# Optimization experiments

Measured on AMD Instinct MI355X. Metric: run time of the kernel, lower is better.

Reference implementation:

```python
import jax, jax.numpy as jnp
import numpy as np

N = 100000   # nodes
E = 3200000  # edges
F = 128      # num_features
H = 20       # hidden dim (hard-coded in source)
C = 10       # num_classes
EPS = 1e-5


def setup_inputs() -> dict:
    key = jax.random.key(0)
    ks = jax.random.split(key, 16)
    x = jax.random.normal(ks[0], (N, F), jnp.float32)
    edge_index = jax.random.randint(ks[1], (2, E), 0, N)
    edge_weights = jnp.ones((E,), jnp.float32)

    def lin_init(k, fan_in, shape):
        s = 1.0 / np.sqrt(fan_in)
        return jax.random.uniform(k, shape, jnp.float32, -s, s)

    return {
        "x": x,
        "edge_index": edge_index,
        "edge_weights": edge_weights,
        "W1": lin_init(ks[2], F, (F, H)), "b1": jnp.zeros((H,), jnp.float32),
        "g1": jnp.ones((H,), jnp.float32), "be1": jnp.zeros((H,), jnp.float32),
        "W2": lin_init(ks[3], H, (H, H)), "b2": jnp.zeros((H,), jnp.float32),
        "g2": jnp.ones((H,), jnp.float32), "be2": jnp.zeros((H,), jnp.float32),
        "W3": lin_init(ks[4], H, (H, H)), "b3": jnp.zeros((H,), jnp.float32),
        "Wl": lin_init(ks[5], 3 * H, (3 * H, C)), "bl": lin_init(ks[6], 3 * H, (C,)),
    }


def gcn_conv(x, src, dst, ew, W, b, n):
    # PyG GCNConv: transform, add self-loops, symmetric deg^-1/2 normalization, scatter-add.
    h = x @ W  # [N, out]
    loop = jnp.arange(n)
    src2 = jnp.concatenate([src, loop])
    dst2 = jnp.concatenate([dst, loop])
    ew2 = jnp.concatenate([ew, jnp.ones((n,), x.dtype)])
    deg = jax.ops.segment_sum(ew2, dst2, num_segments=n)
    dinv = jnp.where(deg > 0, jax.lax.rsqrt(deg), 0.0)
    coef = (dinv[src2] * ew2 * dinv[dst2])[:, None]  # [E+N, 1]
    out = jax.ops.segment_sum(h[src2] * coef, dst2, num_segments=n)
    return out + b


def batch_norm(x, g, b):
    m = x.mean(axis=0)
    v = x.var(axis=0)
    return (x - m) * jax.lax.rsqrt(v + EPS) * g + b


def reference(x, edge_index, edge_weights, W1, b1, g1, be1, W2, b2, g2, be2, W3, b3, Wl, bl):
    src, dst = edge_index[0], edge_index[1]
    n = x.shape[0]
    o1 = batch_norm(jax.nn.relu(gcn_conv(x, src, dst, edge_weights, W1, b1, n)), g1, be1)
    o2 = batch_norm(jax.nn.relu(gcn_conv(o1, src, dst, edge_weights, W2, b2, n)), g2, be2)
    o3 = jax.nn.relu(gcn_conv(o2, src, dst, edge_weights, W3, b3, n))
    emb = jnp.concatenate([o1, o2, o3], axis=1)  # [N, 60]
    return emb @ Wl + bl
```

## Files before the change

kernel.cpp:

```cpp
#include <hip/hip_runtime.h>
#include <hip/hip_fp16.h>


#define HD 20
#define EPS 1e-5f
#define BSH 7
#define NBMAX 1024
#define CAP 5632
#define CAPE 2816

typedef float __attribute__((ext_vector_type(4))) f4v;

__device__ __forceinline__ float4 ntld4(const float* p) {
    f4v v = __builtin_nontemporal_load((const f4v*)p);
    return make_float4(v.x, v.y, v.z, v.w);
}

__global__ __launch_bounds__(1024)
void init_kernel(int* bcnt, float* stats, float* zero20, int nbv) {
    int t = threadIdx.x;
    if (t < nbv) bcnt[t] = 0;
    if (t < 80) stats[t] = 0.0f;
    if (t < HD) zero20[t] = 0.0f;
}

__global__ __launch_bounds__(256)
void bucket_hist_kernel(const int* __restrict__ dst, int* __restrict__ bcnt,
                        int E, int chunk, int nbv) {
    __shared__ int lh[NBMAX];
    for (int i = threadIdx.x; i < nbv; i += 256) lh[i] = 0;
    __syncthreads();
    int s = blockIdx.x * chunk;
    int e = s + chunk; if (e > E) e = E;
    for (int j = s + threadIdx.x; j < e; j += 256)
        atomicAdd(&lh[dst[j] >> BSH], 1);
    __syncthreads();
    for (int i = threadIdx.x; i < nbv; i += 256)
        if (lh[i]) atomicAdd(&bcnt[i], lh[i]);
}

__global__ __launch_bounds__(1024)
void bucket_scan_kernel(const int* __restrict__ bcnt, int* __restrict__ bstart,
                        int* __restrict__ bcur, int* __restrict__ row_start,
                        int n, int E, int nbv) {
    __shared__ int s[1024];
    int t = threadIdx.x;
    int v = (t < nbv) ? bcnt[t] : 0;
    s[t] = v;
    __syncthreads();
    for (int off = 1; off < 1024; off <<= 1) {
        int u = (t >= off) ? s[t - off] : 0;
        __syncthreads();
        s[t] += u;
        __syncthreads();
    }
    if (t < nbv) { int st = s[t] - v; bstart[t] = st; bcur[t] = st; }
    if (t == 0) { bstart[nbv] = E; row_start[n] = E; }
}

__global__ __launch_bounds__(256)
void scatter_kernel(const int* __restrict__ src, const int* __restrict__ dst,
                    const float* __restrict__ ew, int* __restrict__ bcur,
                    int2* __restrict__ tmp, int E, int chunk, int nbv) {
    __shared__ int lh[NBMAX];
    __shared__ int lbase[NBMAX];
    for (int i = threadIdx.x; i < nbv; i += 256) lh[i] = 0;
    __syncthreads();
    int s = blockIdx.x * chunk;
    int e = s + chunk; if (e > E) e = E;
    for (int j = s + threadIdx.x; j < e; j += 256)
        atomicAdd(&lh[dst[j] >> BSH], 1);
    __syncthreads();
    for (int i = threadIdx.x; i < nbv; i += 256) {
        int c = lh[i];
        lbase[i] = c ? atomicAdd(&bcur[i], c) : 0;
        lh[i] = 0;
    }
    __syncthreads();
    for (int j = s + threadIdx.x; j < e; j += 256) {
        int d = dst[j];
        int b = d >> BSH;
        int pos = atomicAdd(&lh[b], 1);
        tmp[lbase[b] + pos] = make_int2(src[j] | ((d & ((1 << BSH) - 1)) << 20),
                                        __float_as_int(ew[j]));
    }
}

__global__ __launch_bounds__(256)
void finalize_kernel(const int2* __restrict__ tmp, const int* __restrict__ bstart,
                     int2* __restrict__ se, int* __restrict__ row_start,
                     float* __restrict__ dinv, int n) {
    __shared__ int hist[128];
    __shared__ float degs[128];
    __shared__ int off[128];
    __shared__ int cur[128];
    __shared__ int2 stage[CAP];
    int b = blockIdx.x;
    int s0 = bstart[b], s1 = bstart[b + 1];
    int cnt = s1 - s0;
    int t = threadIdx.x;
    if (t < 128) { hist[t] = 0; degs[t] = 0.0f; cur[t] = 0; }
    __syncthreads();
    for (int j = s0 + t; j < s1; j += 256) {
        int2 r = tmp[j];
        int l = r.x >> 20;
        atomicAdd(&hist[l], 1);
        atomicAdd(&degs[l], __int_as_float(r.y));
    }
    __syncthreads();
    if (t < 128) off[t] = hist[t];
    __syncthreads();
    for (int o = 1; o < 128; o <<= 1) {
        int u = (t < 128 && t >= o) ? off[t - o] : 0;
        __syncthreads();
        if (t < 128) off[t] += u;
        __syncthreads();
    }
    if (t < 128) {
        int node = (b << BSH) + t;
        if (node < n) {
            row_start[node] = s0 + off[t] - hist[t];
            dinv[node] = rsqrtf(1.0f + degs[t]);
        }
    }
    __syncthreads();
    if (cnt <= CAP) {
        for (int j = s0 + t; j < s1; j += 256) {
            int2 r = tmp[j];
            int l = r.x >> 20;
            int p = (off[l] - hist[l]) + atomicAdd(&cur[l], 1);
            stage[p] = make_int2(r.x & 0xFFFFF, r.y);
        }
        __syncthreads();
        for (int k = t; k < cnt; k += 256) se[s0 + k] = stage[k];
    } else {
        for (int j = s0 + t; j < s1; j += 256) {
            int2 r = tmp[j];
            int l = r.x >> 20;
            int p = (off[l] - hist[l]) + atomicAdd(&cur[l], 1);
            se[s0 + p] = make_int2(r.x & 0xFFFFF, r.y);
        }
    }
}

template<int FIN, int NPB>
__global__ __launch_bounds__(256)
void gemm_kernel(const float* __restrict__ in, const float* __restrict__ W,
                 const float* __restrict__ cvec, const float* __restrict__ dinv,
                 __half* __restrict__ hs, int n) {
    __shared__ float sWt[HD][FIN + 4];
    __shared__ float sIn[NPB][FIN + 4];
    __shared__ float sC[HD];
    for (int i = threadIdx.x; i < FIN * HD; i += 256) {
        int k = i / HD, f = i % HD;
        sWt[f][k] = W[i];
    }
    if (threadIdx.x < HD) sC[threadIdx.x] = cvec[threadIdx.x];
    int base = blockIdx.x * NPB;
    int nb = n - base; if (nb > NPB) nb = NPB;
    int lim = n * FIN;
    const int Q = FIN / 4;
    for (int i = threadIdx.x; i < NPB * Q; i += 256) {
        int row = i / Q, c = (i % Q) * 4;
        int g = (base + row) * FIN + c;
        *(float4*)&sIn[row][c] = (g < lim) ? ntld4(&in[g])
                                           : make_float4(0.f, 0.f, 0.f, 0.f);
    }
    __syncthreads();
    for (int idx = threadIdx.x; idx < NPB * HD; idx += 256) {
        int nl = idx / HD, f = idx % HD;
        float4 a = make_float4(0.f, 0.f, 0.f, 0.f);
        #pragma unroll 4
        for (int k = 0; k < FIN; k += 4) {
            float4 x4 = *(const float4*)&sIn[nl][k];
            float4 w4 = *(const float4*)&sWt[f][k];
            a.x = fmaf(x4.x, w4.x, a.x);
            a.y = fmaf(x4.y, w4.y, a.y);
            a.z = fmaf(x4.z, w4.z, a.z);
            a.w = fmaf(x4.w, w4.w, a.w);
        }
        if (nl < nb)
            hs[(size_t)(base + nl) * HD + f] = __float2half_rn(
                (((a.x + a.y) + (a.z + a.w)) + sC[f]) * dinv[base + nl]);
    }
}

#define FMA4(A, V, W) \
    A.x = fmaf(V.x, W, A.x); A.y = fmaf(V.y, W, A.y); \
    A.z = fmaf(V.z, W, A.z); A.w = fmaf(V.w, W, A.w);

__device__ __forceinline__ float4 h4f2(uint2 u) {
    float2 f0 = __half22float2(*reinterpret_cast<const __half2*>(&u.x));
    float2 f1 = __half22float2(*reinterpret_cast<const __half2*>(&u.y));
    return make_float4(f0.x, f0.y, f1.x, f1.y);
}

#define AGG_LOOP(EDGEAT)                                                     \
    {                                                                        \
        int2 e = EDGEAT(j);                                                  \
        float w = __int_as_float(e.y);                                       \
        const uint2* r = hs4 + (size_t)e.x * 5;                              \
        uint2 c0 = r[0], c1 = r[1], c2 = r[2], c3 = r[3], c4 = r[4];         \
        while (true) {                                                       \
            int jn = j + 4;                                                  \
            bool more = jn < s1;                                             \
            int jp = more ? jn : j;                                          \
            int2 en = EDGEAT(jp);                                            \
            const uint2* rn = hs4 + (size_t)en.x * 5;                        \
            uint2 n0 = rn[0], n1 = rn[1], n2 = rn[2], n3 = rn[3], n4 = rn[4];\
            float wn = __int_as_float(en.y);                                 \
            float4 v0 = h4f2(c0), v1 = h4f2(c1), v2 = h4f2(c2);              \
            float4 v3 = h4f2(c3), v4 = h4f2(c4);                             \
            FMA4(a0, v0, w) FMA4(a1, v1, w) FMA4(a2, v2, w)                  \
            FMA4(a3, v3, w) FMA4(a4, v4, w)                                  \
            if (!more) break;                                                \
            j = jn; w = wn;                                                  \
            c0 = n0; c1 = n1; c2 = n2; c3 = n3; c4 = n4;                     \
        }                                                                    \
    }

#define EDGE_LDS(jj) sse[(jj) - sb0]
#define EDGE_GBL(jj) se[(jj)]

template<int MODE>
__global__ __launch_bounds__(256)
void agg_kernel(const uint2* __restrict__ hs4, const float* __restrict__ dinv,
                const int* __restrict__ row_start, const int2* __restrict__ se,
                const float* __restrict__ bias, float* __restrict__ out,
                float* __restrict__ stat_sum, float* __restrict__ stat_sq,
                const float* __restrict__ o1, const float* __restrict__ o2,
                const float* __restrict__ Wlp, const float* __restrict__ blp,
                int n) {
    __shared__ int2 sse[CAPE];
    __shared__ float ls[HD], lq[HD];
    __shared__ float sW[600];
    __shared__ float sb[10];
    int base = blockIdx.x * 64;
    int nEnd = base + 64; if (nEnd > n) nEnd = n;
    int sb0 = row_start[base];
    int sb1 = row_start[nEnd];
    int span = sb1 - sb0;
    bool ok = (span <= CAPE);
    if (MODE == 0) {
        if (threadIdx.x < HD) { ls[threadIdx.x] = 0.0f; lq[threadIdx.x] = 0.0f; }
    } else {
        for (int i = threadIdx.x; i < 600; i += 256) sW[i] = Wlp[i];
        if (threadIdx.x < 10) sb[threadIdx.x] = blp[threadIdx.x];
    }
    if (ok) {
        for (int k = threadIdx.x; k < span; k += 256) {
            long long v = __builtin_nontemporal_load(
                (const long long*)(se + sb0 + k));
            sse[k] = *(const int2*)&v;
        }
    }
    __syncthreads();
    int i = base + (threadIdx.x >> 2), lane = threadIdx.x & 3;
    if (i < n) {
        float di = dinv[i];
        int s0 = row_start[i], s1 = row_start[i + 1];
        float4 a0, a1, a2, a3, a4;
        if (lane == 0) {
            const uint2* s = hs4 + (size_t)i * 5;
            a0 = h4f2(s[0]); a1 = h4f2(s[1]); a2 = h4f2(s[2]);
            a3 = h4f2(s[3]); a4 = h4f2(s[4]);
        } else {
            a0 = a1 = a2 = a3 = a4 = make_float4(0.f, 0.f, 0.f, 0.f);
        }
        int j = s0 + lane;
        if (j < s1) {
            if (ok) { AGG_LOOP(EDGE_LDS) }
            else    { AGG_LOOP(EDGE_GBL) }
        }
        #define REDX(A, M) \
            A.x += __shfl_xor(A.x, M); A.y += __shfl_xor(A.y, M); \
            A.z += __shfl_xor(A.z, M); A.w += __shfl_xor(A.w, M);
        #define RED4L(A) REDX(A, 1) REDX(A, 2)
        RED4L(a0) RED4L(a1) RED4L(a2) RED4L(a3) RED4L(a4)
        float4 acc[5] = {a0, a1, a2, a3, a4};
        float va[HD];
        #pragma unroll
        for (int q = 0; q < 5; ++q) {
            float4 bb = *(const float4*)(bias + 4 * q);
            va[4 * q + 0] = fmaxf(fmaf(acc[q].x, di, bb.x), 0.0f);
            va[4 * q + 1] = fmaxf(fmaf(acc[q].y, di, bb.y), 0.0f);
            va[4 * q + 2] = fmaxf(fmaf(acc[q].z, di, bb.z), 0.0f);
            va[4 * q + 3] = fmaxf(fmaf(acc[q].w, di, bb.w), 0.0f);
        }
        if (MODE == 0) {
            if (lane == 0) {
                #pragma unroll
                for (int q = 0; q < 5; ++q) {
                    ((float4*)out)[i * 5 + q] = make_float4(
                        va[4 * q], va[4 * q + 1], va[4 * q + 2], va[4 * q + 3]);
                    int f = 4 * q;
                    atomicAdd(&ls[f + 0], va[f + 0]); atomicAdd(&lq[f + 0], va[f + 0] * va[f + 0]);
                    atomicAdd(&ls[f + 1], va[f + 1]); atomicAdd(&lq[f + 1], va[f + 1] * va[f + 1]);
                    atomicAdd(&ls[f + 2], va[f + 2]); atomicAdd(&lq[f + 2], va[f + 2] * va[f + 2]);
                    atomicAdd(&ls[f + 3], va[f + 3]); atomicAdd(&lq[f + 3], va[f + 3] * va[f + 3]);
                }
            }
        } else {
            float r1[HD], r2[HD];
            #pragma unroll
            for (int q = 0; q < 5; ++q) {
                *(float4*)&r1[4 * q] = ((const float4*)(o1 + (size_t)i * HD))[q];
                *(float4*)&r2[4 * q] = ((const float4*)(o2 + (size_t)i * HD))[q];
            }
            for (int c = lane; c < 10; c += 4) {
                float s = sb[c];
                #pragma unroll
                for (int k = 0; k < HD; ++k) s = fmaf(r1[k], sW[k * 10 + c], s);
                #pragma unroll
                for (int k = 0; k < HD; ++k) s = fmaf(r2[k], sW[(HD + k) * 10 + c], s);
                #pragma unroll
                for (int k = 0; k < HD; ++k) s = fmaf(va[k], sW[(2 * HD + k) * 10 + c], s);
                out[(size_t)i * 10 + c] = s;
            }
        }
    }
    if (MODE == 0) {
        __syncthreads();
        if (threadIdx.x < HD) {
            atomicAdd(&stat_sum[threadIdx.x], ls[threadIdx.x]);
            atomicAdd(&stat_sq[threadIdx.x], lq[threadIdx.x]);
        }
    }
}

__global__ __launch_bounds__(512)
void bn_adjust_kernel(const float* __restrict__ sum, const float* __restrict__ sq,
                      const float* __restrict__ g, const float* __restrict__ be,
                      const float* __restrict__ W, float* __restrict__ scsh_out,
                      float* __restrict__ Wp, float* __restrict__ cvec, int n) {
    __shared__ float ssc[HD], ssh[HD];
    int t = threadIdx.x;
    if (t < HD) {
        float inv_n = 1.0f / (float)n;
        float m = sum[t] * inv_n;
        float var = sq[t] * inv_n - m * m;
        float sc = g[t] * rsqrtf(var + EPS);
        float sh = be[t] - m * sc;
        ssc[t] = sc; ssh[t] = sh;
        scsh_out[t] = sc; scsh_out[HD + t] = sh;
    }
    __syncthreads();
    if (t < HD * HD) Wp[t] = ssc[t / HD] * W[t];
    if (t < HD) {
        float acc = 0.0f;
        #pragma unroll
        for (int k = 0; k < HD; ++k) acc = fmaf(ssh[k], W[k * HD + t], acc);
        cvec[t] = acc;
    }
}

__global__ __launch_bounds__(640)
void bn_adjust2_kernel(const float* __restrict__ sum, const float* __restrict__ sq,
                       const float* __restrict__ g, const float* __restrict__ be,
                       const float* __restrict__ W, float* __restrict__ scsh_out,
                       float* __restrict__ Wp, float* __restrict__ cvec,
                       const float* __restrict__ Wl, const float* __restrict__ bl,
                       const float* __restrict__ scsh1,
                       float* __restrict__ Wlp, float* __restrict__ blp, int n) {
    __shared__ float ssc[HD], ssh[HD];
    int t = threadIdx.x;
    if (t < HD) {
        float inv_n = 1.0f / (float)n;
        float m = sum[t] * inv_n;
        float var = sq[t] * inv_n - m * m;
        float sc = g[t] * rsqrtf(var + EPS);
        float sh = be[t] - m * sc;
        ssc[t] = sc; ssh[t] = sh;
        scsh_out[t] = sc; scsh_out[HD + t] = sh;
    }
    __syncthreads();
    if (t < HD * HD) Wp[t] = ssc[t / HD] * W[t];
    if (t < HD) {
        float acc = 0.0f;
        #pragma unroll
        for (int k = 0; k < HD; ++k) acc = fmaf(ssh[k], W[k * HD + t], acc);
        cvec[t] = acc;
    }
    if (t < 600) {
        int k = t / 10;
        float s = (k < HD) ? scsh1[k] : (k < 2 * HD) ? ssc[k - HD] : 1.0f;
        Wlp[t] = s * Wl[t];
    }
    if (t < 10) {
        float acc = bl[t];
        #pragma unroll
        for (int k = 0; k < HD; ++k) acc = fmaf(scsh1[HD + k], Wl[k * 10 + t], acc);
        #pragma unroll
        for (int k = 0; k < HD; ++k) acc = fmaf(ssh[k], Wl[(HD + k) * 10 + t], acc);
        blp[t] = acc;
    }
}

extern "C" void kernel_launch(void* const* d_in, const int* in_sizes, int n_in,
                              void* d_out, int out_size, void* d_ws, size_t ws_size,
                              hipStream_t stream) {
    const float* x   = (const float*)d_in[0];
    const int*   ei  = (const int*)d_in[1];
    const float* ew  = (const float*)d_in[2];
    const float* W1  = (const float*)d_in[3];
    const float* b1  = (const float*)d_in[4];
    const float* g1  = (const float*)d_in[5];
    const float* be1 = (const float*)d_in[6];
    const float* W2  = (const float*)d_in[7];
    const float* b2  = (const float*)d_in[8];
    const float* g2  = (const float*)d_in[9];
    const float* be2 = (const float*)d_in[10];
    const float* W3  = (const float*)d_in[11];
    const float* b3  = (const float*)d_in[12];
    const float* Wl  = (const float*)d_in[13];
    const float* bl  = (const float*)d_in[14];
    float* out = (float*)d_out;

    const int F = in_sizes[3] / HD;
    const int N = in_sizes[0] / F;
    const int E = in_sizes[2];
    const int* src = ei;
    const int* dst = ei + E;
    const int nbv = (N + 127) >> BSH;

    char* p = (char*)d_ws;
    auto alloc = [&](size_t bytes) -> void* {
        void* r = (void*)p;
        p += (bytes + 255) & ~(size_t)255;
        return r;
    };
    size_t nh4 = (size_t)N * HD * 4;
    int2*  se      = (int2*) alloc((size_t)E * 8);
    char*  regionA = (char*) alloc((size_t)E * 8);
    float* o2r     = (float*)alloc(nh4);
    float* dinv    = (float*)alloc((size_t)N * 4);
    int*   row_start = (int*)alloc((size_t)(N + 1) * 4);
    int*   bcnt    = (int*)  alloc(NBMAX * 4);
    int*   bstart  = (int*)  alloc((NBMAX + 1) * 4);
    int*   bcur    = (int*)  alloc(NBMAX * 4);
    float* stats   = (float*)alloc(80 * 4);
    float* scsh    = (float*)alloc(80 * 4);
    float* zero20  = (float*)alloc(20 * 4);
    float* W2p     = (float*)alloc(400 * 4);
    float* c2      = (float*)alloc(20 * 4);
    float* W3p     = (float*)alloc(400 * 4);
    float* c3      = (float*)alloc(20 * 4);
    float* Wlp     = (float*)alloc(600 * 4);
    float* blp     = (float*)alloc(12 * 4);

    int2*   tmp = (int2*)regionA;
    __half* hs  = (__half*)regionA;
    float*  o1r = (float*)(regionA + 2 * nh4);

    const uint2* hs4 = (const uint2*)hs;

    const int B = 256;
    const int GB = 512;
    const int chunk = (E + GB - 1) / GB;
    int gAgg = (4 * N + B - 1) / B;

    hipLaunchKernelGGL(init_kernel, dim3(1), dim3(1024), 0, stream, bcnt, stats, zero20, nbv);
    hipLaunchKernelGGL(bucket_hist_kernel, dim3(GB), dim3(B), 0, stream, dst, bcnt, E, chunk, nbv);
    hipLaunchKernelGGL(bucket_scan_kernel, dim3(1), dim3(1024), 0, stream,
                       bcnt, bstart, bcur, row_start, N, E, nbv);
    hipLaunchKernelGGL(scatter_kernel, dim3(GB), dim3(B), 0, stream,
                       src, dst, ew, bcur, tmp, E, chunk, nbv);
    hipLaunchKernelGGL(finalize_kernel, dim3(nbv), dim3(B), 0, stream,
                       tmp, bstart, se, row_start, dinv, N);

    hipLaunchKernelGGL((gemm_kernel<128, 16>), dim3((N + 15) / 16), dim3(B), 0, stream,
                       x, W1, zero20, dinv, hs, N);
    hipLaunchKernelGGL((agg_kernel<0>), dim3(gAgg), dim3(B), 0, stream,
                       hs4, dinv, row_start, se, b1, o1r,
                       stats, stats + 20, nullptr, nullptr, nullptr, nullptr, N);
    hipLaunchKernelGGL(bn_adjust_kernel, dim3(1), dim3(512), 0, stream,
                       stats, stats + 20, g1, be1, W2, scsh, W2p, c2, N);

    hipLaunchKernelGGL((gemm_kernel<HD, 64>), dim3((N + 63) / 64), dim3(B), 0, stream,
                       o1r, W2p, c2, dinv, hs, N);
    hipLaunchKernelGGL((agg_kernel<0>), dim3(gAgg), dim3(B), 0, stream,
                       hs4, dinv, row_start, se, b2, o2r,
                       stats + 40, stats + 60, nullptr, nullptr, nullptr, nullptr, N);
    hipLaunchKernelGGL(bn_adjust2_kernel, dim3(1), dim3(640), 0, stream,
                       stats + 40, stats + 60, g2, be2, W3, scsh + 40, W3p, c3,
                       Wl, bl, scsh, Wlp, blp, N);

    hipLaunchKernelGGL((gemm_kernel<HD, 64>), dim3((N + 63) / 64), dim3(B), 0, stream,
                       o2r, W3p, c3, dinv, hs, N);
    hipLaunchKernelGGL((agg_kernel<1>), dim3(gAgg), dim3(B), 0, stream,
                       hs4, dinv, row_start, se, b3, out,
                       nullptr, nullptr, o1r, o2r, Wlp, blp, N);
}
```

Measured before the change: 513.3 us.

## Aggregate per 128-node bucket with edge-balanced segments and LDS atomic flush

Replaces the per-node, 4-lanes-per-row aggregation with a per-bucket kernel. Each of 512 threads takes an equal contiguous slice of the bucket's sorted edges, accumulates runs with the same destination in registers, and flushes them into a shared 128x21 accumulator with LDS atomics. Edge records now keep the local destination index packed in the high bits, and the LDS edge cache is enlarged. The goal is to remove load imbalance from variable node degree and the shuffle reductions. The cost is atomic contention at segment boundaries, larger LDS use per block, and fewer, larger blocks.

Result: slower. 589.8 us (+14.9%).

```diff
diff --git a/kernel.cpp b/kernel.cpp
--- a/kernel.cpp
+++ b/kernel.cpp
@@ -7,7 +7,7 @@
 #define BSH 7
 #define NBMAX 1024
 #define CAP 5632
-#define CAPE 2816
+#define CAPE 4800
 
 typedef float __attribute__((ext_vector_type(4))) f4v;
 
@@ -129,7 +129,7 @@
             int2 r = tmp[j];
             int l = r.x >> 20;
             int p = (off[l] - hist[l]) + atomicAdd(&cur[l], 1);
-            stage[p] = make_int2(r.x & 0xFFFFF, r.y);
+            stage[p] = r;
         }
         __syncthreads();
         for (int k = t; k < cnt; k += 256) se[s0 + k] = stage[k];
@@ -138,7 +138,7 @@
             int2 r = tmp[j];
             int l = r.x >> 20;
             int p = (off[l] - hist[l]) + atomicAdd(&cur[l], 1);
-            se[s0 + p] = make_int2(r.x & 0xFFFFF, r.y);
+            se[s0 + p] = r;
         }
     }
 }
@@ -185,145 +185,169 @@
     }
 }
 
-#define FMA4(A, V, W) \
-    A.x = fmaf(V.x, W, A.x); A.y = fmaf(V.y, W, A.y); \
-    A.z = fmaf(V.z, W, A.z); A.w = fmaf(V.w, W, A.w);
-
 __device__ __forceinline__ float4 h4f2(uint2 u) {
     float2 f0 = __half22float2(*reinterpret_cast<const __half2*>(&u.x));
     float2 f1 = __half22float2(*reinterpret_cast<const __half2*>(&u.y));
     return make_float4(f0.x, f0.y, f1.x, f1.y);
 }
 
-#define AGG_LOOP(EDGEAT)                                                     \
+#define ROWLD(Q0, Q1, Q2, SRC) { \
+    const char* rp_ = (const char*)hsb + (size_t)(SRC) * 40; \
+    Q0 = *(const uint4*)rp_; \
+    Q1 = *(const uint4*)(rp_ + 16); \
+    Q2 = *(const uint2*)(rp_ + 32); }
+
+#define ZERO20(A) { _Pragma("unroll") for (int f_ = 0; f_ < HD; ++f_) A[f_] = 0.0f; }
+
+#define FLUSH20(LOC, A) { float* ap_ = &acc[LOC][0]; \
+    _Pragma("unroll") for (int f_ = 0; f_ < HD; ++f_) atomicAdd(ap_ + f_, A[f_]); }
+
+#define ACCUM20(A, C0, C1, C2, W) { \
+    float4 v0_ = h4f2(make_uint2(C0.x, C0.y)); \
+    float4 v1_ = h4f2(make_uint2(C0.z, C0.w)); \
+    float4 v2_ = h4f2(make_uint2(C1.x, C1.y)); \
+    float4 v3_ = h4f2(make_uint2(C1.z, C1.w)); \
+    float4 v4_ = h4f2(C2); \
+    A[0]  = fmaf(v0_.x, W, A[0]);  A[1]  = fmaf(v0_.y, W, A[1]); \
+    A[2]  = fmaf(v0_.z, W, A[2]);  A[3]  = fmaf(v0_.w, W, A[3]); \
+    A[4]  = fmaf(v1_.x, W, A[4]);  A[5]  = fmaf(v1_.y, W, A[5]); \
+    A[6]  = fmaf(v1_.z, W, A[6]);  A[7]  = fmaf(v1_.w, W, A[7]); \
+    A[8]  = fmaf(v2_.x, W, A[8]);  A[9]  = fmaf(v2_.y, W, A[9]); \
+    A[10] = fmaf(v2_.z, W, A[10]); A[11] = fmaf(v2_.w, W, A[11]); \
+    A[12] = fmaf(v3_.x, W, A[12]); A[13] = fmaf(v3_.y, W, A[13]); \
+    A[14] = fmaf(v3_.z, W, A[14]); A[15] = fmaf(v3_.w, W, A[15]); \
+    A[16] = fmaf(v4_.x, W, A[16]); A[17] = fmaf(v4_.y, W, A[17]); \
+    A[18] = fmaf(v4_.z, W, A[18]); A[19] = fmaf(v4_.w, W, A[19]); }
+
+#define SEG_LOOP(EDGEAT)                                                     \
     {                                                                        \
-        int2 e = EDGEAT(j);                                                  \
-        float w = __int_as_float(e.y);                                       \
-        const uint2* r = hs4 + (size_t)e.x * 5;                              \
-        uint2 c0 = r[0], c1 = r[1], c2 = r[2], c3 = r[3], c4 = r[4];         \
+        int k = b0;                                                          \
+        int2 e = EDGEAT(k);                                                  \
+        uint4 c0, c1; uint2 c2; ROWLD(c0, c1, c2, e.x & 0xFFFFF)             \
         while (true) {                                                       \
-            int jn = j + 4;                                                  \
-            bool more = jn < s1;                                             \
-            int jp = more ? jn : j;                                          \
-            int2 en = EDGEAT(jp);                                            \
-            const uint2* rn = hs4 + (size_t)en.x * 5;                        \
-            uint2 n0 = rn[0], n1 = rn[1], n2 = rn[2], n3 = rn[3], n4 = rn[4];\
-            float wn = __int_as_float(en.y);                                 \
-            float4 v0 = h4f2(c0), v1 = h4f2(c1), v2 = h4f2(c2);              \
-            float4 v3 = h4f2(c3), v4 = h4f2(c4);                             \
-            FMA4(a0, v0, w) FMA4(a1, v1, w) FMA4(a2, v2, w)                  \
-            FMA4(a3, v3, w) FMA4(a4, v4, w)                                  \
+            int kn = k + 1;                                                  \
+            bool more = kn < b1;                                             \
+            int2 en = EDGEAT(more ? kn : k);                                 \
+            uint4 n0, n1; uint2 n2; ROWLD(n0, n1, n2, en.x & 0xFFFFF)        \
+            int loc = e.x >> 20;                                             \
+            if (loc != curd) {                                               \
+                if (curd >= 0) FLUSH20(curd, racc)                           \
+                curd = loc;                                                  \
+                ZERO20(racc)                                                 \
+            }                                                                \
+            float w = __int_as_float(e.y);                                   \
+            ACCUM20(racc, c0, c1, c2, w)                                     \
             if (!more) break;                                                \
-            j = jn; w = wn;                                                  \
-            c0 = n0; c1 = n1; c2 = n2; c3 = n3; c4 = n4;                     \
+            k = kn; e = en;                                                  \
+            c0 = n0; c1 = n1; c2 = n2;                                       \
         }                                                                    \
-    }
-
-#define EDGE_LDS(jj) sse[(jj) - sb0]
-#define EDGE_GBL(jj) se[(jj)]
+        if (curd >= 0) FLUSH20(curd, racc)                                   \
+    }
+
+#define EDGE_LDS(kk) sse[(kk)]
+#define EDGE_GBL(kk) se[s0 + (kk)]
 
 template<int MODE>
-__global__ __launch_bounds__(256)
-void agg_kernel(const uint2* __restrict__ hs4, const float* __restrict__ dinv,
-                const int* __restrict__ row_start, const int2* __restrict__ se,
+__global__ __launch_bounds__(512)
+void agg_kernel(const __half* __restrict__ hsb, const float* __restrict__ dinv,
+                const int2* __restrict__ se, const int* __restrict__ bstart,
                 const float* __restrict__ bias, float* __restrict__ out,
                 float* __restrict__ stat_sum, float* __restrict__ stat_sq,
                 const float* __restrict__ o1, const float* __restrict__ o2,
                 const float* __restrict__ Wlp, const float* __restrict__ blp,
                 int n) {
     __shared__ int2 sse[CAPE];
-    __shared__ float ls[HD], lq[HD];
+    __shared__ float acc[128][21];
+    __shared__ float sbias[HD];
     __shared__ float sW[600];
     __shared__ float sb[10];
-    int base = blockIdx.x * 64;
-    int nEnd = base + 64; if (nEnd > n) nEnd = n;
-    int sb0 = row_start[base];
-    int sb1 = row_start[nEnd];
-    int span = sb1 - sb0;
+    int t = threadIdx.x, b = blockIdx.x;
+    int s0 = bstart[b], s1 = bstart[b + 1];
+    int span = s1 - s0;
     bool ok = (span <= CAPE);
-    if (MODE == 0) {
-        if (threadIdx.x < HD) { ls[threadIdx.x] = 0.0f; lq[threadIdx.x] = 0.0f; }
-    } else {
-        for (int i = threadIdx.x; i < 600; i += 256) sW[i] = Wlp[i];
-        if (threadIdx.x < 10) sb[threadIdx.x] = blp[threadIdx.x];
+    for (int i = t; i < 128 * 21; i += 512) ((float*)acc)[i] = 0.0f;
+    if (t < HD) sbias[t] = bias[t];
+    if (MODE == 1) {
+        for (int i = t; i < 600; i += 512) sW[i] = Wlp[i];
+        if (t < 10) sb[t] = blp[t];
     }
     if (ok) {
-        for (int k = threadIdx.x; k < span; k += 256) {
+        for (int k = t; k < span; k += 512) {
             long long v = __builtin_nontemporal_load(
-                (const long long*)(se + sb0 + k));
+                (const long long*)(se + s0 + k));
             sse[k] = *(const int2*)&v;
         }
     }
     __syncthreads();
-    int i = base + (threadIdx.x >> 2), lane = threadIdx.x & 3;
-    if (i < n) {
-        float di = dinv[i];
-        int s0 = row_start[i], s1 = row_start[i + 1];
-        float4 a0, a1, a2, a3, a4;
-        if (lane == 0) {
-            const uint2* s = hs4 + (size_t)i * 5;
-            a0 = h4f2(s[0]); a1 = h4f2(s[1]); a2 = h4f2(s[2]);
-            a3 = h4f2(s[3]); a4 = h4f2(s[4]);
-        } else {
-            a0 = a1 = a2 = a3 = a4 = make_float4(0.f, 0.f, 0.f, 0.f);
-        }
-        int j = s0 + lane;
-        if (j < s1) {
-            if (ok) { AGG_LOOP(EDGE_LDS) }
-            else    { AGG_LOOP(EDGE_GBL) }
-        }
-        #define REDX(A, M) \
-            A.x += __shfl_xor(A.x, M); A.y += __shfl_xor(A.y, M); \
-            A.z += __shfl_xor(A.z, M); A.w += __shfl_xor(A.w, M);
-        #define RED4L(A) REDX(A, 1) REDX(A, 2)
-        RED4L(a0) RED4L(a1) RED4L(a2) RED4L(a3) RED4L(a4)
-        float4 acc[5] = {a0, a1, a2, a3, a4};
-        float va[HD];
-        #pragma unroll
-        for (int q = 0; q < 5; ++q) {
-            float4 bb = *(const float4*)(bias + 4 * q);
-            va[4 * q + 0] = fmaxf(fmaf(acc[q].x, di, bb.x), 0.0f);
-            va[4 * q + 1] = fmaxf(fmaf(acc[q].y, di, bb.y), 0.0f);
-            va[4 * q + 2] = fmaxf(fmaf(acc[q].z, di, bb.z), 0.0f);
-            va[4 * q + 3] = fmaxf(fmaf(acc[q].w, di, bb.w), 0.0f);
-        }
-        if (MODE == 0) {
-            if (lane == 0) {
+
+    int c = ((span + 511) >> 9) | 1;
+    int b0 = t * c;
+    int b1 = b0 + c; if (b1 > span) b1 = span;
+    if (b0 < b1) {
+        float racc[HD];
+        int curd = -1;
+        if (ok) { SEG_LOOP(EDGE_LDS) }
+        else    { SEG_LOOP(EDGE_GBL) }
+    }
+    __syncthreads();
+
+    if (t < 128) {
+        int i = (b << BSH) + t;
+        if (i < n) {
+            float di = dinv[i];
+            uint4 q0, q1; uint2 q2;
+            ROWLD(q0, q1, q2, i)
+            float sf[HD];
+            *(float4*)&sf[0]  = h4f2(make_uint2(q0.x, q0.y));
+            *(float4*)&sf[4]  = h4f2(make_uint2(q0.z, q0.w));
+            *(float4*)&sf[8]  = h4f2(make_uint2(q1.x, q1.y));
+            *(float4*)&sf[12] = h4f2(make_uint2(q1.z, q1.w));
+            *(float4*)&sf[16] = h4f2(q2);
+            float va[HD];
+            #pragma unroll
+            for (int f = 0; f < HD; ++f)
+                va[f] = fmaxf((acc[t][f] + sf[f]) * di + sbias[f], 0.0f);
+            if (MODE == 0) {
+                float4* op = (float4*)(out + (size_t)i * HD);
+                #pragma unroll
+                for (int q = 0; q < 5; ++q)
+                    op[q] = make_float4(va[4*q], va[4*q+1], va[4*q+2], va[4*q+3]);
+                #pragma unroll
+                for (int f = 0; f < HD; ++f) acc[t][f] = va[f];
+            } else {
+                float r1[HD], r2[HD];
+                const float4* p1 = (const float4*)(o1 + (size_t)i * HD);
+                const float4* p2 = (const float4*)(o2 + (size_t)i * HD);
                 #pragma unroll
                 for (int q = 0; q < 5; ++q) {
-                    ((float4*)out)[i * 5 + q] = make_float4(
-                        va[4 * q], va[4 * q + 1], va[4 * q + 2], va[4 * q + 3]);
-                    int f = 4 * q;
-                    atomicAdd(&ls[f + 0], va[f + 0]); atomicAdd(&lq[f + 0], va[f + 0] * va[f + 0]);
-                    atomicAdd(&ls[f + 1], va[f + 1]); atomicAdd(&lq[f + 1], va[f + 1] * va[f + 1]);
-                    atomicAdd(&ls[f + 2], va[f + 2]); atomicAdd(&lq[f + 2], va[f + 2] * va[f + 2]);
-                    atomicAdd(&ls[f + 3], va[f + 3]); atomicAdd(&lq[f + 3], va[f + 3] * va[f + 3]);
+                    *(float4*)&r1[4*q] = p1[q];
+                    *(float4*)&r2[4*q] = p2[q];
+                }
+                #pragma unroll
+                for (int cc = 0; cc < 10; ++cc) {
+                    float s = sb[cc];
+                    #pragma unroll
+                    for (int k = 0; k < HD; ++k) s = fmaf(r1[k], sW[k * 10 + cc], s);
+                    #pragma unroll
+                    for (int k = 0; k < HD; ++k) s = fmaf(r2[k], sW[(HD + k) * 10 + cc], s);
+                    #pragma unroll
+                    for (int k = 0; k < HD; ++k) s = fmaf(va[k], sW[(2 * HD + k) * 10 + cc], s);
+                    out[(size_t)i * 10 + cc] = s;
                 }
             }
-        } else {
-            float r1[HD], r2[HD];
-            #pragma unroll
-            for (int q = 0; q < 5; ++q) {
-                *(float4*)&r1[4 * q] = ((const float4*)(o1 + (size_t)i * HD))[q];
-                *(float4*)&r2[4 * q] = ((const float4*)(o2 + (size_t)i * HD))[q];
-            }
-            for (int c = lane; c < 10; c += 4) {
-                float s = sb[c];
-                #pragma unroll
-                for (int k = 0; k < HD; ++k) s = fmaf(r1[k], sW[k * 10 + c], s);
-                #pragma unroll
-                for (int k = 0; k < HD; ++k) s = fmaf(r2[k], sW[(HD + k) * 10 + c], s);
-                #pragma unroll
-                for (int k = 0; k < HD; ++k) s = fmaf(va[k], sW[(2 * HD + k) * 10 + c], s);
-                out[(size_t)i * 10 + c] = s;
-            }
         }
     }
     if (MODE == 0) {
         __syncthreads();
-        if (threadIdx.x < HD) {
-            atomicAdd(&stat_sum[threadIdx.x], ls[threadIdx.x]);
-            atomicAdd(&stat_sq[threadIdx.x], lq[threadIdx.x]);
+        if (t < HD) {
+            float s = 0.0f, q = 0.0f;
+            #pragma unroll 8
+            for (int nl = 0; nl < 128; ++nl) {
+                float v = acc[nl][t];
+                s += v; q += v * v;
+            }
+            atomicAdd(&stat_sum[t], s);
+            atomicAdd(&stat_sq[t], q);
         }
     }
 }
@@ -452,12 +476,9 @@
     __half* hs  = (__half*)regionA;
     float*  o1r = (float*)(regionA + 2 * nh4);
 
-    const uint2* hs4 = (const uint2*)hs;
-
     const int B = 256;
     const int GB = 512;
     const int chunk = (E + GB - 1) / GB;
-    int gAgg = (4 * N + B - 1) / B;
 
     hipLaunchKernelGGL(init_kernel, dim3(1), dim3(1024), 0, stream, bcnt, stats, zero20, nbv);
     hipLaunchKernelGGL(bucket_hist_kernel, dim3(GB), dim3(B), 0, stream, dst, bcnt, E, chunk, nbv);
@@ -470,16 +491,16 @@
 
     hipLaunchKernelGGL((gemm_kernel<128, 16>), dim3((N + 15) / 16), dim3(B), 0, stream,
                        x, W1, zero20, dinv, hs, N);
-    hipLaunchKernelGGL((agg_kernel<0>), dim3(gAgg), dim3(B), 0, stream,
-                       hs4, dinv, row_start, se, b1, o1r,
+    hipLaunchKernelGGL((agg_kernel<0>), dim3(nbv), dim3(512), 0, stream,
+                       hs, dinv, se, bstart, b1, o1r,
                        stats, stats + 20, nullptr, nullptr, nullptr, nullptr, N);
     hipLaunchKernelGGL(bn_adjust_kernel, dim3(1), dim3(512), 0, stream,
                        stats, stats + 20, g1, be1, W2, scsh, W2p, c2, N);
 
     hipLaunchKernelGGL((gemm_kernel<HD, 64>), dim3((N + 63) / 64), dim3(B), 0, stream,
                        o1r, W2p, c2, dinv, hs, N);
-    hipLaunchKernelGGL((agg_kernel<0>), dim3(gAgg), dim3(B), 0, stream,
-                       hs4, dinv, row_start, se, b2, o2r,
+    hipLaunchKernelGGL((agg_kernel<0>), dim3(nbv), dim3(512), 0, stream,
+                       hs, dinv, se, bstart, b2, o2r,
                        stats + 40, stats + 60, nullptr, nullptr, nullptr, nullptr, N);
     hipLaunchKernelGGL(bn_adjust2_kernel, dim3(1), dim3(640), 0, stream,
                        stats + 40, stats + 60, g2, be2, W3, scsh + 40, W3p, c3,
@@ -487,7 +508,7 @@
 
     hipLaunchKernelGGL((gemm_kernel<HD, 64>), dim3((N + 63) / 64), dim3(B), 0, stream,
                        o2r, W3p, c3, dinv, hs, N);
-    hipLaunchKernelGGL((agg_kernel<1>), dim3(gAgg), dim3(B), 0, stream,
-                       hs4, dinv, row_start, se, b3, out,
+    hipLaunchKernelGGL((agg_kernel<1>), dim3(nbv), dim3(512), 0, stream,
+                       hs, dinv, se, bstart, b3, out,
                        nullptr, nullptr, o1r, o2r, Wlp, blp, N);
 }
```

## Split half-precision hidden rows into 16+4 arrays and deepen gather prefetch

Applied to the files above, without the earlier changes.

The 20-wide fp16 node features are now stored as two arrays: a 32-byte-aligned 16-element part and a separate 4-element part. Each neighbor gather becomes two 16-byte loads plus one 8-byte load instead of five 8-byte loads, so the gathered rows fall on cache-line boundaries. The aggregation loop also keeps three edges of row loads in flight instead of one, to hide random-gather latency. This costs more registers per thread, which may lower occupancy, and each row now touches two separate memory regions.

Measured after the change: 581.1 us. 13.2% more time.

```diff
diff --git a/kernel.cpp b/kernel.cpp
--- a/kernel.cpp
+++ b/kernel.cpp
@@ -147,7 +147,7 @@
 __global__ __launch_bounds__(256)
 void gemm_kernel(const float* __restrict__ in, const float* __restrict__ W,
                  const float* __restrict__ cvec, const float* __restrict__ dinv,
-                 __half* __restrict__ hs, int n) {
+                 __half* __restrict__ hsA, __half* __restrict__ hsB, int n) {
     __shared__ float sWt[HD][FIN + 4];
     __shared__ float sIn[NPB][FIN + 4];
     __shared__ float sC[HD];
@@ -179,9 +179,12 @@
             a.z = fmaf(x4.z, w4.z, a.z);
             a.w = fmaf(x4.w, w4.w, a.w);
         }
-        if (nl < nb)
-            hs[(size_t)(base + nl) * HD + f] = __float2half_rn(
+        if (nl < nb) {
+            __half hv = __float2half_rn(
                 (((a.x + a.y) + (a.z + a.w)) + sC[f]) * dinv[base + nl]);
+            if (f < 16) hsA[(size_t)(base + nl) * 16 + f] = hv;
+            else        hsB[(size_t)(base + nl) * 4 + (f - 16)] = hv;
+        }
     }
 }
 
@@ -195,27 +198,37 @@
     return make_float4(f0.x, f0.y, f1.x, f1.y);
 }
 
+#define ROWLD(Q0, Q1, Q2, SRC) { \
+    const uint4* pa_ = (const uint4*)(hsA + (size_t)(SRC) * 16); \
+    Q0 = pa_[0]; Q1 = pa_[1]; \
+    Q2 = *(const uint2*)(hsB + (size_t)(SRC) * 4); }
+
 #define AGG_LOOP(EDGEAT)                                                     \
     {                                                                        \
-        int2 e = EDGEAT(j);                                                  \
-        float w = __int_as_float(e.y);                                       \
-        const uint2* r = hs4 + (size_t)e.x * 5;                              \
-        uint2 c0 = r[0], c1 = r[1], c2 = r[2], c3 = r[3], c4 = r[4];         \
+        int2 e0 = EDGEAT(j);                                                 \
+        uint4 p0_, p1_; uint2 p2_; ROWLD(p0_, p1_, p2_, e0.x)                \
+        int j1 = j + 4; bool v1 = j1 < s1;                                   \
+        int2 e1 = EDGEAT(v1 ? j1 : j);                                       \
+        uint4 q0_, q1_; uint2 q2_; ROWLD(q0_, q1_, q2_, e1.x)                \
+        int j2 = j1 + 4; bool v2 = j2 < s1;                                  \
+        int2 e2 = EDGEAT(v2 ? j2 : j);                                       \
+        uint4 r0_, r1_; uint2 r2_; ROWLD(r0_, r1_, r2_, e2.x)                \
         while (true) {                                                       \
-            int jn = j + 4;                                                  \
-            bool more = jn < s1;                                             \
-            int jp = more ? jn : j;                                          \
-            int2 en = EDGEAT(jp);                                            \
-            const uint2* rn = hs4 + (size_t)en.x * 5;                        \
-            uint2 n0 = rn[0], n1 = rn[1], n2 = rn[2], n3 = rn[3], n4 = rn[4];\
-            float wn = __int_as_float(en.y);                                 \
-            float4 v0 = h4f2(c0), v1 = h4f2(c1), v2 = h4f2(c2);              \
-            float4 v3 = h4f2(c3), v4 = h4f2(c4);                             \
-            FMA4(a0, v0, w) FMA4(a1, v1, w) FMA4(a2, v2, w)                  \
-            FMA4(a3, v3, w) FMA4(a4, v4, w)                                  \
-            if (!more) break;                                                \
-            j = jn; w = wn;                                                  \
-            c0 = n0; c1 = n1; c2 = n2; c3 = n3; c4 = n4;                     \
+            int j3 = j2 + 4; bool v3 = j3 < s1;                              \
+            int2 e3 = EDGEAT(v3 ? j3 : j);                                   \
+            uint4 s0_, s1_; uint2 s2_; ROWLD(s0_, s1_, s2_, e3.x)            \
+            float w = __int_as_float(e0.y);                                  \
+            float4 u0 = h4f2(make_uint2(p0_.x, p0_.y));                      \
+            float4 u1 = h4f2(make_uint2(p0_.z, p0_.w));                      \
+            float4 u2 = h4f2(make_uint2(p1_.x, p1_.y));                      \
+            float4 u3 = h4f2(make_uint2(p1_.z, p1_.w));                      \
+            float4 u4 = h4f2(p2_);                                           \
+            FMA4(a0, u0, w) FMA4(a1, u1, w) FMA4(a2, u2, w)                  \
+            FMA4(a3, u3, w) FMA4(a4, u4, w)                                  \
+            if (!v1) break;                                                  \
+            e0 = e1; p0_ = q0_; p1_ = q1_; p2_ = q2_;                        \
+            e1 = e2; q0_ = r0_; q1_ = r1_; q2_ = r2_; v1 = v2;               \
+            e2 = e3; r0_ = s0_; r1_ = s1_; r2_ = s2_; v2 = v3; j2 = j3;      \
         }                                                                    \
     }
 
@@ -224,7 +237,8 @@
 
 template<int MODE>
 __global__ __launch_bounds__(256)
-void agg_kernel(const uint2* __restrict__ hs4, const float* __restrict__ dinv,
+void agg_kernel(const __half* __restrict__ hsA, const __half* __restrict__ hsB,
+                const float* __restrict__ dinv,
                 const int* __restrict__ row_start, const int2* __restrict__ se,
                 const float* __restrict__ bias, float* __restrict__ out,
                 float* __restrict__ stat_sum, float* __restrict__ stat_sq,
@@ -261,9 +275,13 @@
         int s0 = row_start[i], s1 = row_start[i + 1];
         float4 a0, a1, a2, a3, a4;
         if (lane == 0) {
-            const uint2* s = hs4 + (size_t)i * 5;
-            a0 = h4f2(s[0]); a1 = h4f2(s[1]); a2 = h4f2(s[2]);
-            a3 = h4f2(s[3]); a4 = h4f2(s[4]);
+            uint4 y0, y1; uint2 y2;
+            ROWLD(y0, y1, y2, i)
+            a0 = h4f2(make_uint2(y0.x, y0.y));
+            a1 = h4f2(make_uint2(y0.z, y0.w));
+            a2 = h4f2(make_uint2(y1.x, y1.y));
+            a3 = h4f2(make_uint2(y1.z, y1.w));
+            a4 = h4f2(y2);
         } else {
             a0 = a1 = a2 = a3 = a4 = make_float4(0.f, 0.f, 0.f, 0.f);
         }
@@ -449,10 +467,9 @@
     float* blp     = (float*)alloc(12 * 4);
 
     int2*   tmp = (int2*)regionA;
-    __half* hs  = (__half*)regionA;
+    __half* hsA = (__half*)regionA;
+    __half* hsB = (__half*)(regionA + (size_t)N * 32);
     float*  o1r = (float*)(regionA + 2 * nh4);
-
-    const uint2* hs4 = (const uint2*)hs;
 
     const int B = 256;
     const int GB = 512;
@@ -469,25 +486,25 @@
                        tmp, bstart, se, row_start, dinv, N);
 
     hipLaunchKernelGGL((gemm_kernel<128, 16>), dim3((N + 15) / 16), dim3(B), 0, stream,
-                       x, W1, zero20, dinv, hs, N);
+                       x, W1, zero20, dinv, hsA, hsB, N);
     hipLaunchKernelGGL((agg_kernel<0>), dim3(gAgg), dim3(B), 0, stream,
-                       hs4, dinv, row_start, se, b1, o1r,
+                       hsA, hsB, dinv, row_start, se, b1, o1r,
                        stats, stats + 20, nullptr, nullptr, nullptr, nullptr, N);
     hipLaunchKernelGGL(bn_adjust_kernel, dim3(1), dim3(512), 0, stream,
                        stats, stats + 20, g1, be1, W2, scsh, W2p, c2, N);
 
     hipLaunchKernelGGL((gemm_kernel<HD, 64>), dim3((N + 63) / 64), dim3(B), 0, stream,
-                       o1r, W2p, c2, dinv, hs, N);
+                       o1r, W2p, c2, dinv, hsA, hsB, N);
     hipLaunchKernelGGL((agg_kernel<0>), dim3(gAgg), dim3(B), 0, stream,
-                       hs4, dinv, row_start, se, b2, o2r,
+                       hsA, hsB, dinv, row_start, se, b2, o2r,
                        stats + 40, stats + 60, nullptr, nullptr, nullptr, nullptr, N);
     hipLaunchKernelGGL(bn_adjust2_kernel, dim3(1), dim3(640), 0, stream,
                        stats + 40, stats + 60, g2, be2, W3, scsh + 40, W3p, c3,
                        Wl, bl, scsh, Wlp, blp, N);
 
     hipLaunchKernelGGL((gemm_kernel<HD, 64>), dim3((N + 63) / 64), dim3(B), 0, stream,
-                       o2r, W3p, c3, dinv, hs, N);
+                       o2r, W3p, c3, dinv, hsA, hsB, N);
     hipLaunchKernelGGL((agg_kernel<1>), dim3(gAgg), dim3(B), 0, stream,
-                       hs4, dinv, row_start, se, b3, out,
+                       hsA, hsB, dinv, row_start, se, b3, out,
                        nullptr, nullptr, o1r, o2r, Wlp, blp, N);
 }
```
